# Kernel tuning notes

Hardware: AMD Instinct MI355X
Metric: run time of the kernel (lower is better)

The kernel has to match this reference:

```python
import jax, jax.numpy as jnp
import numpy as np

B, T, W, L, H = 32, 1024, 512, 12, 8
CH = W // H                      # per-head dim = 64
IN_CH = 3 + 6 + T                # x + params + class embedding channels = 1033
DFF = 4 * W
NEG = -100000.0
SCALE = 1.0 / np.sqrt(np.sqrt(CH))


def _layernorm(x, g, b, eps=1e-5):
    m = jnp.mean(x, axis=-1, keepdims=True)
    v = jnp.mean(jnp.square(x - m), axis=-1, keepdims=True)
    return (x - m) * jax.lax.rsqrt(v + eps) * g + b


def setup_inputs() -> dict:
    key = jax.random.key(0)
    ks = jax.random.split(key, 40)
    std = 0.25 * np.sqrt(1.0 / W)  # init_scale used inside Transformer

    def n(k, shape, s=std):
        return (jax.random.normal(k, shape, jnp.float32) * s).astype(jnp.float32)

    inp = {
        'x': jax.random.normal(ks[0], (B, 3, T), jnp.float32),
        'params': jax.random.normal(ks[1], (B, 6, T), jnp.float32),
        'mask': (jax.random.uniform(ks[2], (B, T)) > 0.2).astype(jnp.float32),
        'class_emb': jax.random.normal(ks[3], (T, T), jnp.float32),  # nn.Embedding(n_ctx, n_ctx)
        'w_in': n(ks[4], (IN_CH, W), 0.02), 'b_in': jnp.zeros((W,), jnp.float32),
        'ln_pre_g': jnp.ones((W,), jnp.float32), 'ln_pre_b': jnp.zeros((W,), jnp.float32),
        'qkv_w': n(ks[5], (L, W, 3 * W)), 'qkv_b': jnp.zeros((L, 3 * W), jnp.float32),
        'attn_pw': n(ks[6], (L, W, W)), 'attn_pb': jnp.zeros((L, W), jnp.float32),
        'ln1_g': jnp.ones((L, W), jnp.float32), 'ln1_b': jnp.zeros((L, W), jnp.float32),
        'fc_w': n(ks[7], (L, W, DFF)), 'fc_b': jnp.zeros((L, DFF), jnp.float32),
        'fcp_w': n(ks[8], (L, DFF, W)), 'fcp_b': jnp.zeros((L, W), jnp.float32),
        'ln2_g': jnp.ones((L, W), jnp.float32), 'ln2_b': jnp.zeros((L, W), jnp.float32),
        'ln_post_g': jnp.ones((W,), jnp.float32), 'ln_post_b': jnp.zeros((W,), jnp.float32),
        'w_out': n(ks[9], (W, W), 0.02), 'b_out': jnp.zeros((W,), jnp.float32),
        'agg_fc_w': n(ks[10], (W, DFF)), 'agg_fc_b': jnp.zeros((DFF,), jnp.float32),
        'agg_pw': n(ks[11], (DFF, W)), 'agg_pb': jnp.zeros((W,), jnp.float32),
    }
    return inp


def _block(h, p):
    qw, qb, pw, pb, l1g, l1b, fw, fb, gw, gb, l2g, l2b = p
    hn = _layernorm(h, l1g, l1b)
    qkv = (hn @ qw + qb).reshape(B, T, H, 3 * CH)
    q, k, v = jnp.split(qkv, 3, axis=-1)
    att = jnp.einsum('bthc,bshc->bhts', q * SCALE, k * SCALE)
    att = jax.nn.softmax(att.astype(jnp.float32), axis=-1)  # softmax in fp32
    o = jnp.einsum('bhts,bshc->bthc', att, v).reshape(B, T, W)
    h = h + o @ pw + pb
    hn2 = _layernorm(h, l2g, l2b)
    h = h + jax.nn.gelu(hn2 @ fw + fb, approximate=False) @ gw + gb
    return h, None


def reference(x, params, mask, class_emb, w_in, b_in, ln_pre_g, ln_pre_b,
              qkv_w, qkv_b, attn_pw, attn_pb, ln1_g, ln1_b, fc_w, fc_b,
              fcp_w, fcp_b, ln2_g, ln2_b, ln_post_g, ln_post_b, w_out, b_out,
              agg_fc_w, agg_fc_b, agg_pw, agg_pb):
    # concatenate params and class-embedding channels: [B, 1033, T]
    ce = jnp.broadcast_to(class_emb.T[None], (B, T, T))  # class_embed.transpose(1,2)
    xin = jnp.concatenate([x, params, ce], axis=1)
    h = jnp.einsum('bct,cw->btw', xin, w_in) + b_in      # input_proj on [B,T,1033]
    h = _layernorm(h, ln_pre_g, ln_pre_b)
    h, _ = jax.lax.scan(_block, h,
                        (qkv_w, qkv_b, attn_pw, attn_pb, ln1_g, ln1_b,
                         fc_w, fc_b, fcp_w, fcp_b, ln2_g, ln2_b))
    h = _layernorm(h, ln_post_g, ln_post_b)
    h = (h @ w_out + b_out).transpose(0, 2, 1)           # [B, 512, T]
    h = h * mask[:, None, :]
    pooled = jnp.max(h + (1.0 - mask[:, None, :]) * NEG, axis=2)  # [B, 512]
    z = jax.nn.gelu(pooled @ agg_fc_w + agg_fc_b, approximate=False) @ agg_pw + agg_pb
    return (z, h)
```

## Files before the change

kernel.cpp:

```cpp
#include <hip/hip_runtime.h>
#include <hip/hip_bf16.h>


typedef unsigned short u16;
typedef unsigned int u32;
typedef __attribute__((ext_vector_type(8))) short bf16x8;
typedef __attribute__((ext_vector_type(8))) unsigned short us8;
typedef __attribute__((ext_vector_type(4))) unsigned short us4;
typedef __attribute__((ext_vector_type(4))) float f32x4;

__device__ __forceinline__ float bf2f(u16 s) {
  union { u32 u; float f; } c; c.u = ((u32)s) << 16; return c.f;
}
__device__ __forceinline__ u16 f2bf(float f) {
  __hip_bfloat16 h = __float2bfloat16(f);
  union { __hip_bfloat16 h; u16 u; } c; c.h = h; return c.u;
}
__device__ __forceinline__ float gelu_f(float v) {
  return 0.5f * v * (1.0f + erff(v * 0.7071067811865475f));
}
__device__ __forceinline__ void gl2lds16(const u16* g, u16* l) {
  __builtin_amdgcn_global_load_lds((const __attribute__((address_space(1))) void*)g,
                                   (__attribute__((address_space(3))) void*)l, 16, 0, 0);
}
__device__ __forceinline__ f32x4 mfma16(bf16x8 a, bf16x8 b, f32x4 c) {
  return __builtin_amdgcn_mfma_f32_16x16x32_bf16(a, b, c, 0, 0, 0);
}
__device__ __forceinline__ int swz(int row) { return (row ^ (row >> 3)) & 7; }

template <int EPI>
__global__ __launch_bounds__(512)
void gemm_bt(const u16* __restrict__ A, const u16* __restrict__ Bt,
             const float* __restrict__ bias, float* __restrict__ Cf,
             u16* __restrict__ Cb, u16* __restrict__ Vt, int K, int lda, int ldb, int ldc)
{
  __shared__ __align__(16) u16 As[2][256 * 32];
  __shared__ __align__(16) u16 Bs[2][128 * 32];
  const int tid = threadIdx.x;
  const int lane = tid & 63, wid = tid >> 6;
  const int wm = wid & 3, wn = wid >> 2;
  const int nbx = gridDim.x;
  const int nwg = nbx * gridDim.y;
  int lin = blockIdx.y * nbx + blockIdx.x;
  lin = (lin & 7) * (nwg >> 3) + (lin >> 3);
  const long m0 = (long)(lin / nbx) * 256, n0 = (long)(lin % nbx) * 128;

  const int c0 = tid, c1 = tid + 512;
  const int kc0 = (c0 & 3) ^ (((c0 >> 2) >> 1) & 3);
  const int kc1 = (c1 & 3) ^ (((c1 >> 2) >> 1) & 3);
  const int kcb = (tid & 3) ^ (((tid >> 2) >> 1) & 3);
  const u16* aS0 = A + (m0 + (c0 >> 2)) * (long)lda + kc0 * 8;
  const u16* aS1 = A + (m0 + (c1 >> 2)) * (long)lda + kc1 * 8;
  const u16* bS0 = Bt + (n0 + (tid >> 2)) * (long)ldb + kcb * 8;

  f32x4 acc[4][4] = {};
  const int cl4 = lane & 15;
  const int gph = ((lane >> 4) ^ ((cl4 >> 1) & 3)) * 8;
  const int aro = (wm * 64 + cl4) * 32 + gph;
  const int bro = (wn * 64 + cl4) * 32 + gph;
  const int nt = K >> 5;

#define STAGE_AB(buf, k0_)                          \
  gl2lds16(aS0 + (k0_), As[buf] + c0 * 8);          \
  gl2lds16(aS1 + (k0_), As[buf] + c1 * 8);          \
  gl2lds16(bS0 + (k0_), Bs[buf] + tid * 8);

  STAGE_AB(0, 0);
  for (int t = 0; t < nt; ++t) {
    const int cur = t & 1;
    if (t < nt - 1) {
      STAGE_AB(cur ^ 1, (t + 1) * 32);
      asm volatile("s_waitcnt vmcnt(3)" ::: "memory");
    } else {
      asm volatile("s_waitcnt vmcnt(0)" ::: "memory");
    }
    __builtin_amdgcn_s_barrier();
    bf16x8 af[4], bfr[4];
#pragma unroll
    for (int i = 0; i < 4; ++i) af[i] = *(const bf16x8*)(As[cur] + aro + i * 16 * 32);
#pragma unroll
    for (int j = 0; j < 4; ++j) bfr[j] = *(const bf16x8*)(Bs[cur] + bro + j * 16 * 32);
    __builtin_amdgcn_s_setprio(1);
#pragma unroll
    for (int i = 0; i < 4; ++i)
#pragma unroll
      for (int j = 0; j < 4; ++j)
        acc[i][j] = mfma16(af[i], bfr[j], acc[i][j]);
    __builtin_amdgcn_s_setprio(0);
    __builtin_amdgcn_s_barrier();
  }
#undef STAGE_AB
  const int rg = (lane >> 4) * 4, cl = lane & 15;
#pragma unroll
  for (int i = 0; i < 4; ++i) {
#pragma unroll
    for (int j = 0; j < 4; ++j) {
      const long row = m0 + wm * 64 + i * 16 + rg;
      const long col = n0 + wn * 64 + j * 16 + cl;
      const float bv = bias ? bias[col] : 0.0f;
      if (EPI == 4) {
        const int hh = (int)col / 192, off = (int)col - hh * 192;
        if (off < 128) {
#pragma unroll
          for (int r = 0; r < 4; ++r)
            Cb[(row + r) * ldc + col] = f2bf(acc[i][j][r] + bv);
        } else {
          us4 pk;
#pragma unroll
          for (int r = 0; r < 4; ++r) pk[r] = f2bf(acc[i][j][r] + bv);
          const long bl = row >> 10, t0 = row & 1023;
          *(us4*)(Vt + (((bl * 8 + hh) * 64 + (off - 128)) << 10) + t0) = pk;
        }
      } else {
#pragma unroll
        for (int r = 0; r < 4; ++r) {
          float v = acc[i][j][r] + bv;
          long idx = (row + r) * ldc + col;
          if (EPI == 0) Cf[idx] = v;
          else if (EPI == 1) Cb[idx] = f2bf(v);
          else if (EPI == 2) Cf[idx] += v;
          else Cb[idx] = f2bf(gelu_f(v));
        }
      }
    }
  }
}

template <int EPI>
__global__ __launch_bounds__(256)
void gemm_bt1(const u16* __restrict__ A, const u16* __restrict__ Bt,
              const float* __restrict__ bias, float* __restrict__ Cf,
              u16* __restrict__ Cb, int K, int lda, int ldb, int ldc)
{
  __shared__ __align__(16) u16 As[2][128 * 32];
  __shared__ __align__(16) u16 Bs[2][128 * 32];
  const int tid = threadIdx.x;
  const int lane = tid & 63, wid = tid >> 6;
  const int wm = wid >> 1, wn = wid & 1;
  const int nbx = gridDim.x;
  const int nwg = nbx * gridDim.y;
  int lin = blockIdx.y * nbx + blockIdx.x;
  lin = (lin & 7) * (nwg >> 3) + (lin >> 3);
  const long m0 = (long)(lin / nbx) * 128, n0 = (long)(lin % nbx) * 128;

  const int c0 = tid, c1 = tid + 256;
  const int kc0 = (c0 & 3) ^ (((c0 >> 2) >> 1) & 3);
  const int kc1 = (c1 & 3) ^ (((c1 >> 2) >> 1) & 3);
  const u16* aS0 = A + (m0 + (c0 >> 2)) * (long)lda + kc0 * 8;
  const u16* aS1 = A + (m0 + (c1 >> 2)) * (long)lda + kc1 * 8;
  const u16* bS0 = Bt + (n0 + (c0 >> 2)) * (long)ldb + kc0 * 8;
  const u16* bS1 = Bt + (n0 + (c1 >> 2)) * (long)ldb + kc1 * 8;

  f32x4 acc[4][4] = {};
  const int cl4 = lane & 15;
  const int gph = ((lane >> 4) ^ ((cl4 >> 1) & 3)) * 8;
  const int aro = (wm * 64 + cl4) * 32 + gph;
  const int bro = (wn * 64 + cl4) * 32 + gph;
  const int nt = K >> 5;

#define STAGE_AB1(buf, k0_)                         \
  gl2lds16(aS0 + (k0_), As[buf] + c0 * 8);          \
  gl2lds16(aS1 + (k0_), As[buf] + c1 * 8);          \
  gl2lds16(bS0 + (k0_), Bs[buf] + c0 * 8);          \
  gl2lds16(bS1 + (k0_), Bs[buf] + c1 * 8);

  STAGE_AB1(0, 0);
  for (int t = 0; t < nt; ++t) {
    const int cur = t & 1;
    if (t < nt - 1) {
      STAGE_AB1(cur ^ 1, (t + 1) * 32);
      asm volatile("s_waitcnt vmcnt(4)" ::: "memory");
    } else {
      asm volatile("s_waitcnt vmcnt(0)" ::: "memory");
    }
    __builtin_amdgcn_s_barrier();
    bf16x8 af[4], bfr[4];
#pragma unroll
    for (int i = 0; i < 4; ++i) af[i] = *(const bf16x8*)(As[cur] + aro + i * 16 * 32);
#pragma unroll
    for (int j = 0; j < 4; ++j) bfr[j] = *(const bf16x8*)(Bs[cur] + bro + j * 16 * 32);
    __builtin_amdgcn_s_setprio(1);
#pragma unroll
    for (int i = 0; i < 4; ++i)
#pragma unroll
      for (int j = 0; j < 4; ++j)
        acc[i][j] = mfma16(af[i], bfr[j], acc[i][j]);
    __builtin_amdgcn_s_setprio(0);
    __builtin_amdgcn_s_barrier();
  }
#undef STAGE_AB1
  const int rg = (lane >> 4) * 4, cl = lane & 15;
#pragma unroll
  for (int i = 0; i < 4; ++i) {
#pragma unroll
    for (int j = 0; j < 4; ++j) {
      const long row = m0 + wm * 64 + i * 16 + rg;
      const long col = n0 + wn * 64 + j * 16 + cl;
      const float bv = bias ? bias[col] : 0.0f;
#pragma unroll
      for (int r = 0; r < 4; ++r) {
        float v = acc[i][j][r] + bv;
        long idx = (row + r) * ldc + col;
        if (EPI == 0) Cf[idx] = v;
        else if (EPI == 1) Cb[idx] = f2bf(v);
        else if (EPI == 2) Cf[idx] += v;
        else Cb[idx] = f2bf(gelu_f(v));
      }
    }
  }
}

template <int EPI>
__global__ __launch_bounds__(1024)
void gemm_bt2(const u16* __restrict__ A, const u16* __restrict__ Bt,
              const float* __restrict__ bias, float* __restrict__ Cf,
              u16* __restrict__ Cb, int K, int lda, int ldb, int ldc)
{
  __shared__ __align__(16) u16 As[2][256 * 32];
  __shared__ __align__(16) u16 Bs[2][256 * 32];
  const int tid = threadIdx.x;
  const int lane = tid & 63, wid = tid >> 6;
  const int wm = wid & 3, wn = wid >> 2;
  const int nbx = gridDim.x;
  const int nwg = nbx * gridDim.y;
  int lin = blockIdx.y * nbx + blockIdx.x;
  lin = (lin & 7) * (nwg >> 3) + (lin >> 3);
  const long m0 = (long)(lin / nbx) * 256, n0 = (long)(lin % nbx) * 256;

  const int kcA = (tid & 3) ^ (((tid >> 2) >> 1) & 3);
  const u16* aS0 = A + (m0 + (tid >> 2)) * (long)lda + kcA * 8;
  const u16* bS0 = Bt + (n0 + (tid >> 2)) * (long)ldb + kcA * 8;

  f32x4 acc[4][4] = {};
  const int cl4 = lane & 15;
  const int gph = ((lane >> 4) ^ ((cl4 >> 1) & 3)) * 8;
  const int aro = (wm * 64 + cl4) * 32 + gph;
  const int bro = (wn * 64 + cl4) * 32 + gph;
  const int nt = K >> 5;

#define STAGE_AB2(buf, k0_)                         \
  gl2lds16(aS0 + (k0_), As[buf] + tid * 8);         \
  gl2lds16(bS0 + (k0_), Bs[buf] + tid * 8);

  STAGE_AB2(0, 0);
  for (int t = 0; t < nt; ++t) {
    const int cur = t & 1;
    if (t < nt - 1) {
      STAGE_AB2(cur ^ 1, (t + 1) * 32);
      asm volatile("s_waitcnt vmcnt(2)" ::: "memory");
    } else {
      asm volatile("s_waitcnt vmcnt(0)" ::: "memory");
    }
    __builtin_amdgcn_s_barrier();
    bf16x8 af[4], bfr[4];
#pragma unroll
    for (int i = 0; i < 4; ++i) af[i] = *(const bf16x8*)(As[cur] + aro + i * 16 * 32);
#pragma unroll
    for (int j = 0; j < 4; ++j) bfr[j] = *(const bf16x8*)(Bs[cur] + bro + j * 16 * 32);
    __builtin_amdgcn_s_setprio(1);
#pragma unroll
    for (int i = 0; i < 4; ++i)
#pragma unroll
      for (int j = 0; j < 4; ++j)
        acc[i][j] = mfma16(af[i], bfr[j], acc[i][j]);
    __builtin_amdgcn_s_setprio(0);
    __builtin_amdgcn_s_barrier();
  }
#undef STAGE_AB2
  const int rg = (lane >> 4) * 4, cl = lane & 15;
#pragma unroll
  for (int i = 0; i < 4; ++i) {
#pragma unroll
    for (int j = 0; j < 4; ++j) {
      const long row = m0 + wm * 64 + i * 16 + rg;
      const long col = n0 + wn * 64 + j * 16 + cl;
      const float bv = bias ? bias[col] : 0.0f;
#pragma unroll
      for (int r = 0; r < 4; ++r) {
        float v = acc[i][j][r] + bv;
        long idx = (row + r) * ldc + col;
        if (EPI == 0) Cf[idx] = v;
        else if (EPI == 1) Cb[idx] = f2bf(v);
        else if (EPI == 2) Cf[idx] += v;
        else Cb[idx] = f2bf(gelu_f(v));
      }
    }
  }
}

__global__ __launch_bounds__(512)
void attn_k(const u16* __restrict__ qkv, const u16* __restrict__ vt, u16* __restrict__ o)
{
  __shared__ __align__(16) u16 Ks[2][64 * 64];
  __shared__ __align__(16) u16 Vts[2][64 * 64];
  __shared__ __align__(16) u16 Ps[8][512];
  const int tid = threadIdx.x, lane = tid & 63, wid = tid >> 6;
  int lin = blockIdx.x;
  lin = (lin & 7) * 128 + (lin >> 3);
  const int qt = lin & 7, hh = (lin >> 3) & 7, b = lin >> 6;
  const long rowbase = (long)b * 1024;
  const long vbase = (((long)b * 8 + hh) * 64) * 1024;
  const int g = lane >> 4, cl = lane & 15;
  u16* Psw = Ps[wid];
  const int Rq = wid * 16 + cl;
  const int sw2 = ((cl >> 1) & 3) << 3;

  bf16x8 aq[2];
  {
    const u16* qp = qkv + (rowbase + qt * 128 + Rq) * 1536 + hh * 192 + g * 8;
    aq[0] = *(const bf16x8*)(qp);
    aq[1] = *(const bf16x8*)(qp + 32);
  }
#define STAGE_KV(buf, kt_)                                                            \
  {                                                                                   \
    int row = tid >> 3, c8s = (tid & 7) ^ swz(row);                                   \
    gl2lds16(qkv + (rowbase + (kt_) * 64 + row) * 1536 + hh * 192 + 64 + c8s * 8,     \
             Ks[buf] + tid * 8);                                                      \
    gl2lds16(vt + vbase + (long)row * 1024 + (kt_) * 64 + c8s * 8, Vts[buf] + tid * 8); \
  }
  STAGE_KV(0, 0);

  float m = -3.0e38f, l = 0.f;
  f32x4 oacc[4] = {};

  for (int kt = 0; kt < 16; ++kt) {
    const int cur = kt & 1;
    if (kt < 15) {
      STAGE_KV(cur ^ 1, kt + 1);
      asm volatile("s_waitcnt vmcnt(2)" ::: "memory");
    } else {
      asm volatile("s_waitcnt vmcnt(0)" ::: "memory");
    }
    __builtin_amdgcn_s_barrier();
    f32x4 s[4] = {};
    __builtin_amdgcn_s_setprio(1);
#pragma unroll
    for (int j = 0; j < 4; ++j) {
      const int Rk = j * 16 + cl, sk = swz(Rk) << 3;
#pragma unroll
      for (int kb = 0; kb < 2; ++kb) {
        bf16x8 bk = *(const bf16x8*)(Ks[cur] + Rk * 64 + ((kb * 32 + g * 8) ^ sk));
        s[j] = mfma16(bk, aq[kb], s[j]);
      }
    }
    __builtin_amdgcn_s_setprio(0);
    float mx = s[0][0];
#pragma unroll
    for (int j = 0; j < 4; ++j)
#pragma unroll
      for (int r = 0; r < 4; ++r) mx = fmaxf(mx, s[j][r]);
    mx *= 0.125f;
    mx = fmaxf(mx, __shfl_xor(mx, 16, 64));
    mx = fmaxf(mx, __shfl_xor(mx, 32, 64));
    if (!__all(mx <= m + 8.f)) {
      const float mnew = fmaxf(m, mx);
      const float al = __expf(m - mnew);
      m = mnew;
      l *= al;
      float alr[4];
#pragma unroll
      for (int r = 0; r < 4; ++r) alr[r] = __shfl(al, (lane & 48) | (g * 4 + r), 64);
#pragma unroll
      for (int cb = 0; cb < 4; ++cb) {
        f32x4 t = oacc[cb];
        t[0] *= alr[0]; t[1] *= alr[1]; t[2] *= alr[2]; t[3] *= alr[3];
        oacc[cb] = t;
      }
    }
    float p[4][4], ts = 0.f;
#pragma unroll
    for (int j = 0; j < 4; ++j)
#pragma unroll
      for (int r = 0; r < 4; ++r) {
        p[j][r] = __expf(s[j][r] * 0.125f - m);
        ts += p[j][r];
      }
    ts += __shfl_xor(ts, 16, 64);
    ts += __shfl_xor(ts, 32, 64);
    l += ts;
#pragma unroll
    for (int kb = 0; kb < 2; ++kb) {
#pragma unroll
      for (int jj = 0; jj < 2; ++jj) {
        us4 pk;
        pk[0] = f2bf(p[2 * kb + jj][0]); pk[1] = f2bf(p[2 * kb + jj][1]);
        pk[2] = f2bf(p[2 * kb + jj][2]); pk[3] = f2bf(p[2 * kb + jj][3]);
        *(us4*)(&Psw[cl * 32 + ((jj * 16 + g * 4) ^ sw2)]) = pk;
      }
      asm volatile("s_waitcnt lgkmcnt(0)" ::: "memory");
      bf16x8 pa = *(const bf16x8*)(&Psw[cl * 32 + ((g * 8) ^ sw2)]);
      __builtin_amdgcn_s_setprio(1);
#pragma unroll
      for (int cb = 0; cb < 4; ++cb) {
        const int ch = cb * 16 + cl;
        bf16x8 vb = *(const bf16x8*)(Vts[cur] + ch * 64 + ((kb * 32 + g * 8) ^ (swz(ch) << 3)));
        oacc[cb] = mfma16(pa, vb, oacc[cb]);
      }
      __builtin_amdgcn_s_setprio(0);
    }
    __builtin_amdgcn_s_barrier();
  }
#undef STAGE_KV
  float lr[4];
#pragma unroll
  for (int r = 0; r < 4; ++r) lr[r] = __shfl(l, (lane & 48) | (g * 4 + r), 64);
#pragma unroll
  for (int cb = 0; cb < 4; ++cb)
#pragma unroll
    for (int r = 0; r < 4; ++r) {
      long row = rowbase + qt * 128 + wid * 16 + g * 4 + r;
      o[row * 512 + hh * 64 + cb * 16 + cl] = f2bf(oacc[cb][r] / lr[r]);
    }
}

template <int MODE>
__global__ __launch_bounds__(256)
void ln_k(const float* __restrict__ in_, const float* __restrict__ gg,
          const float* __restrict__ bb, void* __restrict__ out_)
{
  const long row = (long)blockIdx.x * 4 + (threadIdx.x >> 6);
  const int lane = threadIdx.x & 63;
  float x[8];
  const float* p = in_ + row * 512 + lane * 8;
  *(float4*)(x) = *(const float4*)(p);
  *(float4*)(x + 4) = *(const float4*)(p + 4);
  float s = 0.f;
#pragma unroll
  for (int j = 0; j < 8; ++j) s += x[j];
#pragma unroll
  for (int off = 1; off < 64; off <<= 1) s += __shfl_xor(s, off, 64);
  const float mean = s * (1.0f / 512.0f);
  float vs = 0.f;
#pragma unroll
  for (int j = 0; j < 8; ++j) { float d = x[j] - mean; vs += d * d; }
#pragma unroll
  for (int off = 1; off < 64; off <<= 1) vs += __shfl_xor(vs, off, 64);
  const float rstd = rsqrtf(vs * (1.0f / 512.0f) + 1e-5f);
  if (MODE == 0) {
    float y[8];
#pragma unroll
    for (int j = 0; j < 8; ++j)
      y[j] = (x[j] - mean) * rstd * gg[lane * 8 + j] + bb[lane * 8 + j];
    float* q = (float*)out_ + row * 512 + lane * 8;
    *(float4*)(q) = *(const float4*)(y);
    *(float4*)(q + 4) = *(const float4*)(y + 4);
  } else {
    us8 ov;
#pragma unroll
    for (int j = 0; j < 8; ++j)
      ov[j] = f2bf((x[j] - mean) * rstd * gg[lane * 8 + j] + bb[lane * 8 + j]);
    *(us8*)((u16*)out_ + row * 512 + lane * 8) = ov;
  }
}

__global__ __launch_bounds__(256)
void embed_k(const float* __restrict__ x, const float* __restrict__ par,
             const float* __restrict__ E, const float* __restrict__ w_in,
             const float* __restrict__ b_in, float* __restrict__ h)
{
  const long bt = blockIdx.x;
  const int b = (int)(bt >> 10), t = (int)(bt & 1023);
  float xs[9];
#pragma unroll
  for (int c = 0; c < 3; ++c) xs[c] = x[((long)b * 3 + c) * 1024 + t];
#pragma unroll
  for (int c = 0; c < 6; ++c) xs[3 + c] = par[((long)b * 6 + c) * 1024 + t];
  for (int w = threadIdx.x; w < 512; w += 256) {
    float a = E[(long)t * 512 + w] + b_in[w];
#pragma unroll
    for (int c = 0; c < 9; ++c) a += xs[c] * w_in[c * 512 + w];
    h[bt * 512 + w] = a;
  }
}

__global__ __launch_bounds__(256)
void tr_k(const float* __restrict__ in, u16* __restrict__ out, int R, int C)
{
  __shared__ u16 tile[32][33];
  const int r0 = blockIdx.y * 32, c0 = blockIdx.x * 32;
  const int tx = threadIdx.x & 31, ty = threadIdx.x >> 5;
  for (int rr = ty; rr < 32; rr += 8) tile[rr][tx] = f2bf(in[(long)(r0 + rr) * C + c0 + tx]);
  __syncthreads();
  for (int rr = ty; rr < 32; rr += 8) out[(long)(c0 + rr) * R + r0 + tx] = tile[tx][rr];
}

__global__ __launch_bounds__(256)
void trL_k(const float* __restrict__ qkv_w, const float* __restrict__ pw,
           const float* __restrict__ fcw, const float* __restrict__ fcpw,
           u16* __restrict__ o_qkv, u16* __restrict__ o_pw,
           u16* __restrict__ o_fc, u16* __restrict__ o_fcp)
{
  __shared__ u16 tile[32][33];
  int bid = blockIdx.x;
  const float* src; u16* dst; int R, C, bx, by;
  if (bid < 768)       { src = qkv_w; dst = o_qkv; R = 512;  C = 1536; bx = bid % 48; by = bid / 48; }
  else if (bid < 1024) { bid -= 768;  src = pw;   dst = o_pw;  R = 512;  C = 512;  bx = bid % 16; by = bid / 16; }
  else if (bid < 2048) { bid -= 1024; src = fcw;  dst = o_fc;  R = 512;  C = 2048; bx = bid % 64; by = bid / 64; }
  else                 { bid -= 2048; src = fcpw; dst = o_fcp; R = 2048; C = 512;  bx = bid % 16; by = bid / 16; }
  const int r0 = by * 32, c0 = bx * 32;
  const int tx = threadIdx.x & 31, ty = threadIdx.x >> 5;
  for (int rr = ty; rr < 32; rr += 8) tile[rr][tx] = f2bf(src[(long)(r0 + rr) * C + c0 + tx]);
  __syncthreads();
  for (int rr = ty; rr < 32; rr += 8) dst[(long)(c0 + rr) * R + r0 + tx] = tile[tx][rr];
}

__global__ __launch_bounds__(256)
void cast_k(const float* __restrict__ in, u16* __restrict__ out, long n)
{
  long i = ((long)blockIdx.x * 256 + threadIdx.x) * 4;
  if (i + 3 < n) {
    float4 v = *(const float4*)(in + i);
    out[i] = f2bf(v.x); out[i + 1] = f2bf(v.y); out[i + 2] = f2bf(v.z); out[i + 3] = f2bf(v.w);
  }
}

__global__ __launch_bounds__(256)
void pool1_k(const float* __restrict__ hm, const float* __restrict__ mask, float* __restrict__ part)
{
  const int c = blockIdx.x, b = blockIdx.y;
  const int t0 = c * 128;
  const int w0 = threadIdx.x, w1 = threadIdx.x + 256;
  float m0 = -3.0e38f, m1 = -3.0e38f;
  for (int t = 0; t < 128; ++t) {
    const float mv = mask[b * 1024 + t0 + t];
    const float neg = (1.0f - mv) * (-100000.0f);
    const float* row = hm + ((long)b * 1024 + t0 + t) * 512;
    m0 = fmaxf(m0, row[w0] * mv + neg);
    m1 = fmaxf(m1, row[w1] * mv + neg);
  }
  part[((long)b * 8 + c) * 512 + w0] = m0;
  part[((long)b * 8 + c) * 512 + w1] = m1;
}
__global__ __launch_bounds__(256)
void pool2_k(const float* __restrict__ part, float* __restrict__ pooled)
{
  const int b = blockIdx.y;
  const int w = blockIdx.x * 256 + threadIdx.x;
  float m = -3.0e38f;
#pragma unroll
  for (int c = 0; c < 8; ++c) m = fmaxf(m, part[((long)b * 8 + c) * 512 + w]);
  pooled[b * 512 + w] = m;
}

__global__ __launch_bounds__(256)
void tout_k(const float* __restrict__ hm, const float* __restrict__ mask, float* __restrict__ outh)
{
  __shared__ float tile[64][65];
  const int t0 = blockIdx.x * 64, w0 = blockIdx.y * 64, b = blockIdx.z;
  const int tx = threadIdx.x & 63, ty = threadIdx.x >> 6;
  for (int i = ty; i < 64; i += 4)
    tile[i][tx] = hm[((long)b * 1024 + t0 + i) * 512 + w0 + tx];
  __syncthreads();
  const float mv = mask[b * 1024 + t0 + tx];
  for (int i = ty; i < 64; i += 4)
    outh[((long)b * 512 + w0 + i) * 1024 + t0 + tx] = tile[tx][i] * mv;
}

__global__ __launch_bounds__(256)
void agg1p_k(const float* __restrict__ pooled, const float* __restrict__ wf,
             float* __restrict__ part)
{
  const int b = blockIdx.z, kc = blockIdx.y;
  const int n = blockIdx.x * 256 + threadIdx.x;
  float acc = 0.f;
  const int k0 = kc * 64;
#pragma unroll 8
  for (int k = 0; k < 64; ++k) acc += pooled[b * 512 + k0 + k] * wf[(long)(k0 + k) * 2048 + n];
  part[((long)b * 8 + kc) * 2048 + n] = acc;
}
__global__ __launch_bounds__(256)
void agg1c_k(const float* __restrict__ part, const float* __restrict__ bf_,
             float* __restrict__ z1)
{
  const int b = blockIdx.y;
  const int n = blockIdx.x * 256 + threadIdx.x;
  float acc = 0.f;
#pragma unroll
  for (int c = 0; c < 8; ++c) acc += part[((long)b * 8 + c) * 2048 + n];
  z1[(long)b * 2048 + n] = gelu_f(acc + bf_[n]);
}
__global__ __launch_bounds__(256)
void agg2p_k(const float* __restrict__ z1, const float* __restrict__ wp,
             float* __restrict__ part)
{
  const int b = blockIdx.z, kc = blockIdx.y;
  const int n = blockIdx.x * 256 + threadIdx.x;
  float acc = 0.f;
  const int k0 = kc * 256;
#pragma unroll 8
  for (int k = 0; k < 256; ++k) acc += z1[(long)b * 2048 + k0 + k] * wp[(long)(k0 + k) * 512 + n];
  part[((long)b * 8 + kc) * 512 + n] = acc;
}
__global__ __launch_bounds__(256)
void agg2c_k(const float* __restrict__ part, const float* __restrict__ bp,
             float* __restrict__ zo)
{
  const int b = blockIdx.y;
  const int n = blockIdx.x * 256 + threadIdx.x;
  float acc = 0.f;
#pragma unroll
  for (int c = 0; c < 8; ++c) acc += part[((long)b * 8 + c) * 512 + n];
  zo[b * 512 + n] = acc + bp[n];
}

extern "C" void kernel_launch(void* const* d_in, const int* in_sizes, int n_in,
                              void* d_out, int out_size, void* d_ws, size_t ws_size,
                              hipStream_t stream)
{
  (void)in_sizes; (void)n_in; (void)out_size; (void)ws_size;
  const float* x        = (const float*)d_in[0];
  const float* params   = (const float*)d_in[1];
  const float* mask     = (const float*)d_in[2];
  const float* class_emb= (const float*)d_in[3];
  const float* w_in     = (const float*)d_in[4];
  const float* b_in     = (const float*)d_in[5];
  const float* ln_pre_g = (const float*)d_in[6];
  const float* ln_pre_b = (const float*)d_in[7];
  const float* qkv_w    = (const float*)d_in[8];
  const float* qkv_b    = (const float*)d_in[9];
  const float* attn_pw  = (const float*)d_in[10];
  const float* attn_pb  = (const float*)d_in[11];
  const float* ln1_g    = (const float*)d_in[12];
  const float* ln1_b    = (const float*)d_in[13];
  const float* fc_w     = (const float*)d_in[14];
  const float* fc_b     = (const float*)d_in[15];
  const float* fcp_w    = (const float*)d_in[16];
  const float* fcp_b    = (const float*)d_in[17];
  const float* ln2_g    = (const float*)d_in[18];
  const float* ln2_b    = (const float*)d_in[19];
  const float* ln_post_g= (const float*)d_in[20];
  const float* ln_post_b= (const float*)d_in[21];
  const float* w_out    = (const float*)d_in[22];
  const float* b_out    = (const float*)d_in[23];
  const float* agg_fc_w = (const float*)d_in[24];
  const float* agg_fc_b = (const float*)d_in[25];
  const float* agg_pw   = (const float*)d_in[26];
  const float* agg_pb   = (const float*)d_in[27];

  float* out_f = (float*)d_out;
  float* out_h = out_f + 16384;
  u16* sc = (u16*)out_h;

  char* ws = (char*)d_ws;
  float* hf = (float*)ws;       ws += (size_t)32768 * 512 * 4;
  u16* hn = (u16*)ws;           ws += (size_t)32768 * 512 * 2;
  float* E = (float*)ws;        ws += (size_t)1024 * 512 * 4;
  u16* ce_b = (u16*)ws;         ws += (size_t)1024 * 1024 * 2;
  u16* wt_qkv = (u16*)ws;       ws += (size_t)1536 * 512 * 2;
  u16* wt_pw  = (u16*)ws;       ws += (size_t)512 * 512 * 2;
  u16* wt_fc  = (u16*)ws;       ws += (size_t)2048 * 512 * 2;
  u16* wt_fcp = (u16*)ws;       ws += (size_t)512 * 2048 * 2;
  u16* w_in_t = (u16*)ws;       ws += (size_t)512 * 1024 * 2;
  u16* w_out_t= (u16*)ws;       ws += (size_t)512 * 512 * 2;
  float* pooled = (float*)ws;   ws += (size_t)32 * 512 * 4;
  float* z1     = (float*)ws;   ws += (size_t)32 * 2048 * 4;
  float* part   = (float*)ws;   ws += (size_t)32 * 8 * 512 * 4;
  float* apart1 = (float*)ws;   ws += (size_t)32 * 8 * 2048 * 4;
  float* apart2 = (float*)ws;   ws += (size_t)32 * 8 * 512 * 4;
  u16* vt       = (u16*)ws;     ws += (size_t)16 * 8 * 64 * 1024 * 2;

  cast_k<<<1024, 256, 0, stream>>>(class_emb, ce_b, 1024 * 1024);
  tr_k<<<dim3(16, 32), 256, 0, stream>>>(w_in + 9 * 512, w_in_t, 1024, 512);
  tr_k<<<dim3(16, 16), 256, 0, stream>>>(w_out, w_out_t, 512, 512);
  gemm_bt<0><<<dim3(4, 4), 512, 0, stream>>>(ce_b, w_in_t, nullptr, E, nullptr, nullptr,
                                             1024, 1024, 1024, 512);
  embed_k<<<32768, 256, 0, stream>>>(x, params, E, w_in, b_in, hf);
  ln_k<0><<<8192, 256, 0, stream>>>(hf, ln_pre_g, ln_pre_b, hf);

  for (int l = 0; l < 12; ++l) {
    trL_k<<<3072, 256, 0, stream>>>(qkv_w + (size_t)l * 512 * 1536,
                                    attn_pw + (size_t)l * 512 * 512,
                                    fc_w + (size_t)l * 512 * 2048,
                                    fcp_w + (size_t)l * 2048 * 512,
                                    wt_qkv, wt_pw, wt_fc, wt_fcp);

    ln_k<1><<<8192, 256, 0, stream>>>(hf, ln1_g + l * 512, ln1_b + l * 512, hn);
    for (int half = 0; half < 2; ++half) {
      const size_t ro = (size_t)half * 16384;
      gemm_bt<4><<<dim3(12, 64), 512, 0, stream>>>(hn + ro * 512, wt_qkv, qkv_b + l * 1536,
                                                   nullptr, sc, vt, 512, 512, 512, 1536);
      attn_k<<<1024, 512, 0, stream>>>(sc, vt, hn + ro * 512);
    }
    gemm_bt<2><<<dim3(4, 128), 512, 0, stream>>>(hn, wt_pw, attn_pb + l * 512,
                                                 hf, nullptr, nullptr, 512, 512, 512, 512);
    ln_k<1><<<8192, 256, 0, stream>>>(hf, ln2_g + l * 512, ln2_b + l * 512, hn);
    for (int half = 0; half < 2; ++half) {
      const size_t ro = (size_t)half * 16384;
      gemm_bt2<3><<<dim3(8, 64), 1024, 0, stream>>>(hn + ro * 512, wt_fc, fc_b + l * 2048,
                                                    nullptr, sc, 512, 512, 512, 2048);
      gemm_bt1<2><<<dim3(4, 128), 256, 0, stream>>>(sc, wt_fcp, fcp_b + l * 512,
                                                    hf + ro * 512, nullptr, 2048, 2048, 2048, 512);
    }
  }

  ln_k<1><<<8192, 256, 0, stream>>>(hf, ln_post_g, ln_post_b, hn);
  gemm_bt<0><<<dim3(4, 128), 512, 0, stream>>>(hn, w_out_t, b_out, hf, nullptr, nullptr,
                                               512, 512, 512, 512);
  pool1_k<<<dim3(8, 32), 256, 0, stream>>>(hf, mask, part);
  pool2_k<<<dim3(2, 32), 256, 0, stream>>>(part, pooled);
  agg1p_k<<<dim3(8, 8, 32), 256, 0, stream>>>(pooled, agg_fc_w, apart1);
  agg1c_k<<<dim3(8, 32), 256, 0, stream>>>(apart1, agg_fc_b, z1);
  agg2p_k<<<dim3(2, 8, 32), 256, 0, stream>>>(z1, agg_pw, apart2);
  agg2c_k<<<dim3(2, 32), 256, 0, stream>>>(apart2, agg_pb, out_f);
  tout_k<<<dim3(16, 8, 32), 256, 0, stream>>>(hf, mask, out_h);
}
```

Baseline: 6.436 ms.

## Fold softmax scale into Q, fuse embed+LN and pooling into transpose, swap GEMM kernels

The 1/8 attention scale now multiplies Q in the QKV GEMM epilogue, so the attention inner loop skips it. The input embedding and pre-LayerNorm become one kernel, and the masked max-pool is computed inside the output transpose, replacing the separate pool1 pass. The attention projection and output GEMMs switch to the gemm_bt1 variant with a different grid. Scaling Q before bf16 rounding changes rounding slightly, and the fused pool uses 16 partials instead of 8.

```diff
diff --git a/kernel.cpp b/kernel.cpp
--- a/kernel.cpp
+++ b/kernel.cpp
@@ -100,7 +100,11 @@
       const float bv = bias ? bias[col] : 0.0f;
       if (EPI == 4) {
         const int hh = (int)col / 192, off = (int)col - hh * 192;
-        if (off < 128) {
+        if (off < 64) {
+#pragma unroll
+          for (int r = 0; r < 4; ++r)
+            Cb[(row + r) * ldc + col] = f2bf((acc[i][j][r] + bv) * 0.125f);
+        } else if (off < 128) {
 #pragma unroll
           for (int r = 0; r < 4; ++r)
             Cb[(row + r) * ldc + col] = f2bf(acc[i][j][r] + bv);
@@ -349,7 +353,6 @@
     for (int j = 0; j < 4; ++j)
 #pragma unroll
       for (int r = 0; r < 4; ++r) mx = fmaxf(mx, s[j][r]);
-    mx *= 0.125f;
     mx = fmaxf(mx, __shfl_xor(mx, 16, 64));
     mx = fmaxf(mx, __shfl_xor(mx, 32, 64));
     if (!__all(mx <= m + 8.f)) {
@@ -372,7 +375,7 @@
     for (int j = 0; j < 4; ++j)
 #pragma unroll
       for (int r = 0; r < 4; ++r) {
-        p[j][r] = __expf(s[j][r] * 0.125f - m);
+        p[j][r] = __expf(s[j][r] - m);
         ts += p[j][r];
       }
     ts += __shfl_xor(ts, 16, 64);
@@ -454,22 +457,46 @@
 }
 
 __global__ __launch_bounds__(256)
-void embed_k(const float* __restrict__ x, const float* __restrict__ par,
-             const float* __restrict__ E, const float* __restrict__ w_in,
-             const float* __restrict__ b_in, float* __restrict__ h)
-{
+void embed_ln_k(const float* __restrict__ x, const float* __restrict__ par,
+                const float* __restrict__ E, const float* __restrict__ w_in,
+                const float* __restrict__ b_in, const float* __restrict__ gg,
+                const float* __restrict__ bb, float* __restrict__ h)
+{
+  __shared__ float red[8];
   const long bt = blockIdx.x;
   const int b = (int)(bt >> 10), t = (int)(bt & 1023);
+  const int tid = threadIdx.x, lane = tid & 63, wid = tid >> 6;
   float xs[9];
 #pragma unroll
   for (int c = 0; c < 3; ++c) xs[c] = x[((long)b * 3 + c) * 1024 + t];
 #pragma unroll
   for (int c = 0; c < 6; ++c) xs[3 + c] = par[((long)b * 6 + c) * 1024 + t];
-  for (int w = threadIdx.x; w < 512; w += 256) {
-    float a = E[(long)t * 512 + w] + b_in[w];
-#pragma unroll
-    for (int c = 0; c < 9; ++c) a += xs[c] * w_in[c * 512 + w];
-    h[bt * 512 + w] = a;
+  float a[2];
+#pragma unroll
+  for (int ii = 0; ii < 2; ++ii) {
+    const int w = tid + ii * 256;
+    float v = E[(long)t * 512 + w] + b_in[w];
+#pragma unroll
+    for (int c = 0; c < 9; ++c) v += xs[c] * w_in[c * 512 + w];
+    a[ii] = v;
+  }
+  float s = a[0] + a[1];
+#pragma unroll
+  for (int off = 1; off < 64; off <<= 1) s += __shfl_xor(s, off, 64);
+  if (lane == 0) red[wid] = s;
+  __syncthreads();
+  const float mean = (red[0] + red[1] + red[2] + red[3]) * (1.0f / 512.0f);
+  float d0 = a[0] - mean, d1 = a[1] - mean;
+  float vs = d0 * d0 + d1 * d1;
+#pragma unroll
+  for (int off = 1; off < 64; off <<= 1) vs += __shfl_xor(vs, off, 64);
+  if (lane == 0) red[4 + wid] = vs;
+  __syncthreads();
+  const float rstd = rsqrtf((red[4] + red[5] + red[6] + red[7]) * (1.0f / 512.0f) + 1e-5f);
+#pragma unroll
+  for (int ii = 0; ii < 2; ++ii) {
+    const int w = tid + ii * 256;
+    h[bt * 512 + w] = (a[ii] - mean) * rstd * gg[w] + bb[w];
   }
 }
 
@@ -515,45 +542,36 @@
 }
 
 __global__ __launch_bounds__(256)
-void pool1_k(const float* __restrict__ hm, const float* __restrict__ mask, float* __restrict__ part)
-{
-  const int c = blockIdx.x, b = blockIdx.y;
-  const int t0 = c * 128;
-  const int w0 = threadIdx.x, w1 = threadIdx.x + 256;
-  float m0 = -3.0e38f, m1 = -3.0e38f;
-  for (int t = 0; t < 128; ++t) {
-    const float mv = mask[b * 1024 + t0 + t];
-    const float neg = (1.0f - mv) * (-100000.0f);
-    const float* row = hm + ((long)b * 1024 + t0 + t) * 512;
-    m0 = fmaxf(m0, row[w0] * mv + neg);
-    m1 = fmaxf(m1, row[w1] * mv + neg);
-  }
-  part[((long)b * 8 + c) * 512 + w0] = m0;
-  part[((long)b * 8 + c) * 512 + w1] = m1;
-}
-__global__ __launch_bounds__(256)
-void pool2_k(const float* __restrict__ part, float* __restrict__ pooled)
-{
-  const int b = blockIdx.y;
-  const int w = blockIdx.x * 256 + threadIdx.x;
-  float m = -3.0e38f;
-#pragma unroll
-  for (int c = 0; c < 8; ++c) m = fmaxf(m, part[((long)b * 8 + c) * 512 + w]);
-  pooled[b * 512 + w] = m;
-}
-
-__global__ __launch_bounds__(256)
-void tout_k(const float* __restrict__ hm, const float* __restrict__ mask, float* __restrict__ outh)
+void tout_k(const float* __restrict__ hm, const float* __restrict__ mask,
+            float* __restrict__ outh, float* __restrict__ part)
 {
   __shared__ float tile[64][65];
-  const int t0 = blockIdx.x * 64, w0 = blockIdx.y * 64, b = blockIdx.z;
+  const int bx = blockIdx.x;
+  const int t0 = bx * 64, w0 = blockIdx.y * 64, b = blockIdx.z;
   const int tx = threadIdx.x & 63, ty = threadIdx.x >> 6;
   for (int i = ty; i < 64; i += 4)
     tile[i][tx] = hm[((long)b * 1024 + t0 + i) * 512 + w0 + tx];
   __syncthreads();
   const float mv = mask[b * 1024 + t0 + tx];
-  for (int i = ty; i < 64; i += 4)
-    outh[((long)b * 512 + w0 + i) * 1024 + t0 + tx] = tile[tx][i] * mv;
+  const float neg = (1.0f - mv) * (-100000.0f);
+  for (int i = ty; i < 64; i += 4) {
+    const float v = tile[tx][i] * mv;
+    outh[((long)b * 512 + w0 + i) * 1024 + t0 + tx] = v;
+    float pm = v + neg;
+#pragma unroll
+    for (int off = 1; off < 64; off <<= 1) pm = fmaxf(pm, __shfl_xor(pm, off, 64));
+    if (tx == 0) part[(((long)b * 16 + bx) * 512) + w0 + i] = pm;
+  }
+}
+__global__ __launch_bounds__(256)
+void pool2_k(const float* __restrict__ part, float* __restrict__ pooled)
+{
+  const int b = blockIdx.y;
+  const int w = blockIdx.x * 256 + threadIdx.x;
+  float m = -3.0e38f;
+#pragma unroll
+  for (int c = 0; c < 16; ++c) m = fmaxf(m, part[((long)b * 16 + c) * 512 + w]);
+  pooled[b * 512 + w] = m;
 }
 
 __global__ __launch_bounds__(256)
@@ -654,7 +672,7 @@
   u16* w_out_t= (u16*)ws;       ws += (size_t)512 * 512 * 2;
   float* pooled = (float*)ws;   ws += (size_t)32 * 512 * 4;
   float* z1     = (float*)ws;   ws += (size_t)32 * 2048 * 4;
-  float* part   = (float*)ws;   ws += (size_t)32 * 8 * 512 * 4;
+  float* part   = (float*)ws;   ws += (size_t)32 * 16 * 512 * 4;
   float* apart1 = (float*)ws;   ws += (size_t)32 * 8 * 2048 * 4;
   float* apart2 = (float*)ws;   ws += (size_t)32 * 8 * 512 * 4;
   u16* vt       = (u16*)ws;     ws += (size_t)16 * 8 * 64 * 1024 * 2;
@@ -664,8 +682,7 @@
   tr_k<<<dim3(16, 16), 256, 0, stream>>>(w_out, w_out_t, 512, 512);
   gemm_bt<0><<<dim3(4, 4), 512, 0, stream>>>(ce_b, w_in_t, nullptr, E, nullptr, nullptr,
                                              1024, 1024, 1024, 512);
-  embed_k<<<32768, 256, 0, stream>>>(x, params, E, w_in, b_in, hf);
-  ln_k<0><<<8192, 256, 0, stream>>>(hf, ln_pre_g, ln_pre_b, hf);
+  embed_ln_k<<<32768, 256, 0, stream>>>(x, params, E, w_in, b_in, ln_pre_g, ln_pre_b, hf);
 
   for (int l = 0; l < 12; ++l) {
     trL_k<<<3072, 256, 0, stream>>>(qkv_w + (size_t)l * 512 * 1536,
@@ -681,8 +698,8 @@
                                                    nullptr, sc, vt, 512, 512, 512, 1536);
       attn_k<<<1024, 512, 0, stream>>>(sc, vt, hn + ro * 512);
     }
-    gemm_bt<2><<<dim3(4, 128), 512, 0, stream>>>(hn, wt_pw, attn_pb + l * 512,
-                                                 hf, nullptr, nullptr, 512, 512, 512, 512);
+    gemm_bt1<2><<<dim3(4, 256), 256, 0, stream>>>(hn, wt_pw, attn_pb + l * 512,
+                                                  hf, nullptr, 512, 512, 512, 512);
     ln_k<1><<<8192, 256, 0, stream>>>(hf, ln2_g + l * 512, ln2_b + l * 512, hn);
     for (int half = 0; half < 2; ++half) {
       const size_t ro = (size_t)half * 16384;
@@ -694,13 +711,12 @@
   }
 
   ln_k<1><<<8192, 256, 0, stream>>>(hf, ln_post_g, ln_post_b, hn);
-  gemm_bt<0><<<dim3(4, 128), 512, 0, stream>>>(hn, w_out_t, b_out, hf, nullptr, nullptr,
-                                               512, 512, 512, 512);
-  pool1_k<<<dim3(8, 32), 256, 0, stream>>>(hf, mask, part);
+  gemm_bt1<0><<<dim3(4, 256), 256, 0, stream>>>(hn, w_out_t, b_out, hf, nullptr,
+                                                512, 512, 512, 512);
+  tout_k<<<dim3(16, 8, 32), 256, 0, stream>>>(hf, mask, out_h, part);
   pool2_k<<<dim3(2, 32), 256, 0, stream>>>(part, pooled);
   agg1p_k<<<dim3(8, 8, 32), 256, 0, stream>>>(pooled, agg_fc_w, apart1);
   agg1c_k<<<dim3(8, 32), 256, 0, stream>>>(apart1, agg_fc_b, z1);
   agg2p_k<<<dim3(2, 8, 32), 256, 0, stream>>>(z1, agg_pw, apart2);
   agg2c_k<<<dim3(2, 32), 256, 0, stream>>>(apart2, agg_pb, out_f);
-  tout_k<<<dim3(16, 8, 32), 256, 0, stream>>>(hf, mask, out_h);
-}
+}
```

Result: slower. 6.678 ms (+3.8%).
